# Optimization experiments

Hardware: AMD Instinct MI355X
Metric: run time of the kernel (lower is better)

The kernel has to match this reference:

```python
import jax, jax.numpy as jnp
import numpy as np

IN_FEATURES = 4096  # 64*64


def setup_inputs() -> dict:
    key = jax.random.key(0)
    kx, k0, k1, k2, k3 = jax.random.split(key, 5)
    u = lambda k, s: jax.random.uniform(k, s, jnp.float32, -0.1, 0.1)
    return {
        "x": jax.random.normal(kx, (8192, 4096), jnp.float32),
        "core0": u(k0, (1, 64, 16)),
        "core1": u(k1, (16, 64, 16)),
        "core2": u(k2, (16, 64, 16)),
        "core3": u(k3, (16, 64, 1)),
    }


def tt_to_matrix(cores, in_features):
    # Sequentially contract TT cores: cores[i] has shape (r_{i-1}, n_i, r_i).
    # Running result: (prod_of_dims_so_far, r_i)
    W = cores[0].reshape(cores[0].shape[1], cores[0].shape[2])  # (n0, r1)
    for c in cores[1:]:
        # (P, r) x (r, n, r') -> (P*n, r')
        W = jnp.einsum("pr,rns->pns", W, c).reshape(-1, c.shape[2])
    return W.reshape(in_features, -1)  # (in_features, out_features)


def reference(x, core0, core1, core2, core3):
    W = tt_to_matrix((core0, core1, core2, core3), IN_FEATURES)  # (4096, 4096)
    return jnp.matmul(x, W)
```

## Files before the change

### kernel.cpp

```cpp
#include <hip/hip_runtime.h>

#define ROWS 8192
#define KDIM 4096
#define NDIM 4096

typedef float f32x4 __attribute__((ext_vector_type(4)));


__device__ inline f32x4 fma4(float s, f32x4 w, f32x4 a) {
    a.x = fmaf(s, w.x, a.x);
    a.y = fmaf(s, w.y, a.y);
    a.z = fmaf(s, w.z, a.z);
    a.w = fmaf(s, w.w, a.w);
    return a;
}
__device__ inline f32x4 shfl_xor4(f32x4 v, int m) {
    v.x = __shfl_xor(v.x, m, 64);
    v.y = __shfl_xor(v.y, m, 64);
    v.z = __shfl_xor(v.z, m, 64);
    v.w = __shfl_xor(v.w, m, 64);
    return v;
}

__global__ __launch_bounds__(256) void tt_prep(
    const float* __restrict__ c0, const float* __restrict__ c1,
    const float* __restrict__ c2, const float* __restrict__ c3,
    float* __restrict__ w01, float* __restrict__ w23)
{
    int gid = blockIdx.x * 256 + threadIdx.x;
    if (gid < 65536) {
        int p = gid >> 4, r2 = gid & 15;
        int n0 = p >> 6, n1 = p & 63;
        float s = 0.f;
        #pragma unroll
        for (int r1 = 0; r1 < 16; ++r1)
            s = fmaf(c0[n0 * 16 + r1], c1[(r1 * 64 + n1) * 16 + r2], s);
        w01[gid] = s;
    } else {
        int g = gid - 65536;
        int r2 = g >> 12, j = g & 4095;
        int n2 = j >> 6, n3 = j & 63;
        float s = 0.f;
        #pragma unroll
        for (int r3 = 0; r3 < 16; ++r3)
            s = fmaf(c2[(r2 * 64 + n2) * 16 + r3], c3[r3 * 64 + n3], s);
        w23[g] = s;
    }
}

__global__ __launch_bounds__(512) void tt_fused(
    const float* __restrict__ x, const float* __restrict__ w01,
    const float* __restrict__ w23, float* __restrict__ out)
{
    __shared__ __align__(16) float tsp[4][16][16];
    __shared__ __align__(16) float ts[16][16];
    const int t = threadIdx.x;
    const int lane = t & 63;
    const int wv = t >> 6;
    const int rg = wv & 1;
    const int ks = wv >> 1;
    const int q = lane & 3;
    const int klane = lane >> 2;
    const int row0 = blockIdx.x * 16 + rg * 8;
    const int k0 = ks * 1024;

    const float* xb = x + (size_t)row0 * KDIM + k0;
    const float* wb = w01 + (size_t)k0 * 16;

    f32x4 acc[8];
    #pragma unroll
    for (int r = 0; r < 8; ++r) acc[r] = (f32x4)(0.f);

    #pragma unroll 2
    for (int it = 0; it < 1024 / 64; ++it) {
        const int kk0 = it * 64 + klane * 4;
        f32x4 wq[4];
        #pragma unroll
        for (int kk = 0; kk < 4; ++kk)
            wq[kk] = *(const f32x4*)&wb[(size_t)(kk0 + kk) * 16 + q * 4];
        f32x4 xv[8];
        #pragma unroll
        for (int r = 0; r < 8; ++r)
            xv[r] = *(const f32x4*)&xb[(size_t)r * KDIM + kk0];
        #pragma unroll
        for (int kk = 0; kk < 4; ++kk)
            #pragma unroll
            for (int r = 0; r < 8; ++r)
                acc[r] = fma4(xv[r][kk], wq[kk], acc[r]);
    }

    const bool b5 = lane & 32, b4 = lane & 16, b3 = lane & 8;
    f32x4 s1[4];
    #pragma unroll
    for (int j = 0; j < 4; ++j) {
        f32x4 send = b5 ? acc[j] : acc[4 + j];
        f32x4 keep = b5 ? acc[4 + j] : acc[j];
        s1[j] = keep + shfl_xor4(send, 32);
    }
    f32x4 s2[2];
    #pragma unroll
    for (int j = 0; j < 2; ++j) {
        f32x4 send = b4 ? s1[j] : s1[2 + j];
        f32x4 keep = b4 ? s1[2 + j] : s1[j];
        s2[j] = keep + shfl_xor4(send, 16);
    }
    f32x4 s3;
    {
        f32x4 send = b3 ? s2[0] : s2[1];
        f32x4 keep = b3 ? s2[1] : s2[0];
        s3 = keep + shfl_xor4(send, 8);
    }
    s3 += shfl_xor4(s3, 4);

    if ((lane & 4) == 0) {
        int row = (lane >> 3) & 7;
        *(f32x4*)&tsp[ks][rg * 8 + row][q * 4] = s3;
    }
    __syncthreads();

    if (t < 256) {
        int row = t >> 4, r = t & 15;
        ts[row][r] = tsp[0][row][r] + tsp[1][row][r]
                   + tsp[2][row][r] + tsp[3][row][r];
    }
    __syncthreads();

    const size_t obase = (size_t)blockIdx.x * 16 * NDIM;
    #pragma unroll 1
    for (int jt = 0; jt < 2; ++jt) {
        const int j0 = jt * 2048 + t * 4;
        f32x4 w[16];
        #pragma unroll
        for (int r = 0; r < 16; ++r)
            w[r] = *(const f32x4*)&w23[r * NDIM + j0];
        #pragma unroll 2
        for (int row = 0; row < 16; ++row) {
            const f32x4* trp = (const f32x4*)&ts[row][0];
            f32x4 t0 = trp[0], t1 = trp[1], t2 = trp[2], t3 = trp[3];
            f32x4 a = (f32x4)(0.f);
            a = fma4(t0.x, w[0],  a); a = fma4(t0.y, w[1],  a);
            a = fma4(t0.z, w[2],  a); a = fma4(t0.w, w[3],  a);
            a = fma4(t1.x, w[4],  a); a = fma4(t1.y, w[5],  a);
            a = fma4(t1.z, w[6],  a); a = fma4(t1.w, w[7],  a);
            a = fma4(t2.x, w[8],  a); a = fma4(t2.y, w[9],  a);
            a = fma4(t2.z, w[10], a); a = fma4(t2.w, w[11], a);
            a = fma4(t3.x, w[12], a); a = fma4(t3.y, w[13], a);
            a = fma4(t3.z, w[14], a); a = fma4(t3.w, w[15], a);
            __builtin_nontemporal_store(a,
                (f32x4*)&out[obase + (size_t)row * NDIM + j0]);
        }
    }
}

extern "C" void kernel_launch(void* const* d_in, const int* in_sizes, int n_in,
                              void* d_out, int out_size, void* d_ws, size_t ws_size,
                              hipStream_t stream) {
    const float* x  = (const float*)d_in[0];
    const float* c0 = (const float*)d_in[1];
    const float* c1 = (const float*)d_in[2];
    const float* c2 = (const float*)d_in[3];
    const float* c3 = (const float*)d_in[4];
    float* out = (float*)d_out;

    float* w01 = (float*)d_ws;
    float* w23 = w01 + 65536;

    tt_prep<<<512, 256, 0, stream>>>(c0, c1, c2, c3, w01, w23);
    tt_fused<<<512, 512, 0, stream>>>(x, w01, w23, out);
}
```

Before: 60.31 us.

## Stage x tiles through LDS with coalesced loads and split K across eight waves

Each wave now handles all 16 rows over a 512-wide K slice, instead of 8 rows over a 1024-wide slice. It loads x in coalesced 128-column chunks into per-wave LDS, then reads it back broadcast-style for the FMA loop. The aim is to replace the strided per-lane 16-byte x loads with contiguous row segments and to reuse each w01 load across 16 rows. This doubles the accumulators, adds a deeper shuffle reduction and adds 64KB of LDS, which may limit occupancy despite the launch-bounds hint.

```diff
diff --git a/kernel.cpp b/kernel.cpp
--- a/kernel.cpp
+++ b/kernel.cpp
@@ -48,84 +48,101 @@
     }
 }
 
-__global__ __launch_bounds__(512) void tt_fused(
+__global__ __launch_bounds__(512, 4) void tt_fused(
     const float* __restrict__ x, const float* __restrict__ w01,
     const float* __restrict__ w23, float* __restrict__ out)
 {
-    __shared__ __align__(16) float tsp[4][16][16];
+    __shared__ __align__(16) float ldsx[8][16][128];
+    __shared__ __align__(16) float tsp[8][16][16];
     __shared__ __align__(16) float ts[16][16];
     const int t = threadIdx.x;
     const int lane = t & 63;
     const int wv = t >> 6;
-    const int rg = wv & 1;
-    const int ks = wv >> 1;
     const int q = lane & 3;
     const int klane = lane >> 2;
-    const int row0 = blockIdx.x * 16 + rg * 8;
-    const int k0 = ks * 1024;
+    const int row0 = blockIdx.x * 16;
+    const int k0 = wv * 512;
+    const int rh = lane >> 5;
+    const int cl = (lane & 31) * 4;
 
     const float* xb = x + (size_t)row0 * KDIM + k0;
     const float* wb = w01 + (size_t)k0 * 16;
 
-    f32x4 acc[8];
+    f32x4 acc[16];
     #pragma unroll
-    for (int r = 0; r < 8; ++r) acc[r] = (f32x4)(0.f);
+    for (int r = 0; r < 16; ++r) acc[r] = (f32x4)(0.f);
 
-    #pragma unroll 2
-    for (int it = 0; it < 1024 / 64; ++it) {
-        const int kk0 = it * 64 + klane * 4;
-        f32x4 wq[4];
+    #pragma unroll 1
+    for (int ch = 0; ch < 4; ++ch) {
+        f32x4 xs[8];
         #pragma unroll
-        for (int kk = 0; kk < 4; ++kk)
-            wq[kk] = *(const f32x4*)&wb[(size_t)(kk0 + kk) * 16 + q * 4];
-        f32x4 xv[8];
+        for (int i = 0; i < 8; ++i)
+            xs[i] = *(const f32x4*)&xb[(size_t)(2 * i + rh) * KDIM + ch * 128 + cl];
         #pragma unroll
-        for (int r = 0; r < 8; ++r)
-            xv[r] = *(const f32x4*)&xb[(size_t)r * KDIM + kk0];
+        for (int i = 0; i < 8; ++i)
+            *(f32x4*)&ldsx[wv][2 * i + rh][cl] = xs[i];
+
         #pragma unroll
-        for (int kk = 0; kk < 4; ++kk)
+        for (int it = 0; it < 2; ++it) {
+            const int kk0 = it * 64 + klane * 4;
+            f32x4 wq[4];
             #pragma unroll
-            for (int r = 0; r < 8; ++r)
-                acc[r] = fma4(xv[r][kk], wq[kk], acc[r]);
+            for (int kk = 0; kk < 4; ++kk)
+                wq[kk] = *(const f32x4*)&wb[(size_t)(ch * 128 + kk0 + kk) * 16 + q * 4];
+            #pragma unroll
+            for (int r = 0; r < 16; ++r) {
+                f32x4 xv = *(const f32x4*)&ldsx[wv][r][kk0];
+                #pragma unroll
+                for (int kk = 0; kk < 4; ++kk)
+                    acc[r] = fma4(xv[kk], wq[kk], acc[r]);
+            }
+        }
     }
 
     const bool b5 = lane & 32, b4 = lane & 16, b3 = lane & 8;
-    f32x4 s1[4];
+    f32x4 s1[8];
+    #pragma unroll
+    for (int j = 0; j < 8; ++j) {
+        f32x4 send = b5 ? acc[j] : acc[8 + j];
+        f32x4 keep = b5 ? acc[8 + j] : acc[j];
+        s1[j] = keep + shfl_xor4(send, 32);
+    }
+    f32x4 s2[4];
     #pragma unroll
     for (int j = 0; j < 4; ++j) {
-        f32x4 send = b5 ? acc[j] : acc[4 + j];
-        f32x4 keep = b5 ? acc[4 + j] : acc[j];
-        s1[j] = keep + shfl_xor4(send, 32);
+        f32x4 send = b4 ? s1[j] : s1[4 + j];
+        f32x4 keep = b4 ? s1[4 + j] : s1[j];
+        s2[j] = keep + shfl_xor4(send, 16);
     }
-    f32x4 s2[2];
+    f32x4 s3[2];
     #pragma unroll
     for (int j = 0; j < 2; ++j) {
-        f32x4 send = b4 ? s1[j] : s1[2 + j];
-        f32x4 keep = b4 ? s1[2 + j] : s1[j];
-        s2[j] = keep + shfl_xor4(send, 16);
+        f32x4 send = b3 ? s2[j] : s2[2 + j];
+        f32x4 keep = b3 ? s2[2 + j] : s2[j];
+        s3[j] = keep + shfl_xor4(send, 8);
     }
-    f32x4 s3;
+    s3[0] += shfl_xor4(s3[0], 4);
+    s3[1] += shfl_xor4(s3[1], 4);
+
     {
-        f32x4 send = b3 ? s2[0] : s2[1];
-        f32x4 keep = b3 ? s2[1] : s2[0];
-        s3 = keep + shfl_xor4(send, 8);
-    }
-    s3 += shfl_xor4(s3, 4);
-
-    if ((lane & 4) == 0) {
-        int row = (lane >> 3) & 7;
-        *(f32x4*)&tsp[ks][rg * 8 + row][q * 4] = s3;
+        f32x4 v = (lane & 4) ? s3[1] : s3[0];
+        int row = ((lane >> 5) & 1) * 8 + ((lane >> 4) & 1) * 4
+                + ((lane >> 3) & 1) * 2 + ((lane >> 2) & 1);
+        *(f32x4*)&tsp[wv][row][q * 4] = v;
     }
     __syncthreads();
 
     if (t < 256) {
         int row = t >> 4, r = t & 15;
-        ts[row][r] = tsp[0][row][r] + tsp[1][row][r]
-                   + tsp[2][row][r] + tsp[3][row][r];
+        float s = 0.f;
+        #pragma unroll
+        for (int w8 = 0; w8 < 8; ++w8)
+            s += tsp[w8][row][r];
+        ts[row][r] = s;
     }
     __syncthreads();
 
-    const size_t obase = (size_t)blockIdx.x * 16 * NDIM;
+    const size_t obase = (size_t)row0 * NDIM;
     #pragma unroll 1
     for (int jt = 0; jt < 2; ++jt) {
         const int j0 = jt * 2048 + t * 4;
```

After: 106.2 us. +76.1%, slower.
